# Kernel tuning notes

Hardware: AMD Instinct MI355X
Metric: run time of the kernel (lower is better)

Reference implementation:

```python
import jax, jax.numpy as jnp
import numpy as np

HID = 2048
HEADS = 16
HEAD_DIM = HID // HEADS  # 128
MLP_HID = 4 * HID
L_IMG = 2048
L_TXT = 256


def _layernorm(x, eps=1e-6):
    mu = jnp.mean(x, axis=-1, keepdims=True)
    xc = x - mu
    var = jnp.mean(xc * xc, axis=-1, keepdims=True)
    return xc * jax.lax.rsqrt(var + eps)


def _rmsnorm(x, scale, eps=1e-6):
    xf = x.astype(jnp.float32)
    rrms = jax.lax.rsqrt(jnp.mean(xf * xf, axis=-1, keepdims=True) + eps)
    return (xf * rrms).astype(x.dtype) * scale


def _apply_rope(x, pe):
    # x: [B,H,L,D], pe: [1,1,L,D/2,2,2]
    B, H, L, D = x.shape
    xf = x.astype(jnp.float32).reshape(B, H, L, D // 2, 1, 2)
    out = pe[..., 0] * xf[..., 0] + pe[..., 1] * xf[..., 1]  # [B,H,L,D/2,2]
    return out.reshape(B, H, L, D).astype(x.dtype)


def _attention(q, k, v, pe):
    q = _apply_rope(q, pe)
    k = _apply_rope(k, pe)
    scale = 1.0 / jnp.sqrt(jnp.float32(q.shape[-1])).astype(q.dtype)
    logits = jnp.einsum('bhqd,bhkd->bhqk', q, k) * scale
    probs = jax.nn.softmax(logits, axis=-1)
    out = jnp.einsum('bhqk,bhkd->bhqd', probs, v)
    B, H, L, D = out.shape
    return out.transpose(0, 2, 1, 3).reshape(B, L, H * D)


def _modulation(vec, w, b):
    out = jnp.dot(jax.nn.silu(vec), w) + b  # [B, 6*dim]
    return jnp.split(out[:, None, :], 6, axis=-1)


def _qkv_heads(x, w, b):
    B, L, _ = x.shape
    qkv = (jnp.dot(x, w) + b).reshape(B, L, 3, HEADS, HEAD_DIM)
    qkv = qkv.transpose(2, 0, 3, 1, 4)  # [3,B,H,L,D]
    return qkv[0], qkv[1], qkv[2]


def _mlp(x, w1, b1, w2, b2):
    return jnp.dot(jax.nn.gelu(jnp.dot(x, w1) + b1, approximate=True), w2) + b2


def setup_inputs() -> dict:
    key = jax.random.key(0)
    ks = iter(jax.random.split(key, 32))
    s = 0.02
    d = {
        'img': jax.random.normal(next(ks), (1, L_IMG, HID), jnp.float32),
        'txt': jax.random.normal(next(ks), (1, L_TXT, HID), jnp.float32),
        'vec': jax.random.normal(next(ks), (1, HID), jnp.float32),
        'pe': jax.random.normal(next(ks), (1, 1, L_TXT + L_IMG, HEAD_DIM // 2, 2, 2), jnp.float32),
    }
    for p in ('img', 'txt'):
        d[p + '_mod_w'] = jax.random.normal(next(ks), (HID, 6 * HID), jnp.float32) * s
        d[p + '_mod_b'] = jnp.zeros((6 * HID,), jnp.float32)
        d[p + '_qkv_w'] = jax.random.normal(next(ks), (HID, 3 * HID), jnp.float32) * s
        d[p + '_qkv_b'] = jnp.zeros((3 * HID,), jnp.float32)
        d[p + '_q_scale'] = jnp.ones((HEAD_DIM,), jnp.float32)
        d[p + '_k_scale'] = jnp.ones((HEAD_DIM,), jnp.float32)
        d[p + '_proj_w'] = jax.random.normal(next(ks), (HID, HID), jnp.float32) * s
        d[p + '_proj_b'] = jnp.zeros((HID,), jnp.float32)
        d[p + '_mlp_w1'] = jax.random.normal(next(ks), (HID, MLP_HID), jnp.float32) * s
        d[p + '_mlp_b1'] = jnp.zeros((MLP_HID,), jnp.float32)
        d[p + '_mlp_w2'] = jax.random.normal(next(ks), (MLP_HID, HID), jnp.float32) * s
        d[p + '_mlp_b2'] = jnp.zeros((HID,), jnp.float32)
    return d


def reference(img, txt, vec, pe,
              img_mod_w, img_mod_b, img_qkv_w, img_qkv_b, img_q_scale, img_k_scale,
              img_proj_w, img_proj_b, img_mlp_w1, img_mlp_b1, img_mlp_w2, img_mlp_b2,
              txt_mod_w, txt_mod_b, txt_qkv_w, txt_qkv_b, txt_q_scale, txt_k_scale,
              txt_proj_w, txt_proj_b, txt_mlp_w1, txt_mlp_b1, txt_mlp_w2, txt_mlp_b2):
    i_sh1, i_sc1, i_g1, i_sh2, i_sc2, i_g2 = _modulation(vec, img_mod_w, img_mod_b)
    t_sh1, t_sc1, t_g1, t_sh2, t_sc2, t_g2 = _modulation(vec, txt_mod_w, txt_mod_b)

    img_modulated = (1 + i_sc1) * _layernorm(img) + i_sh1
    iq, ik, iv = _qkv_heads(img_modulated, img_qkv_w, img_qkv_b)
    iq = _rmsnorm(iq, img_q_scale)
    ik = _rmsnorm(ik, img_k_scale)

    txt_modulated = (1 + t_sc1) * _layernorm(txt) + t_sh1
    tq, tk, tv = _qkv_heads(txt_modulated, txt_qkv_w, txt_qkv_b)
    tq = _rmsnorm(tq, txt_q_scale)
    tk = _rmsnorm(tk, txt_k_scale)

    q = jnp.concatenate((tq, iq), axis=2)
    k = jnp.concatenate((tk, ik), axis=2)
    v = jnp.concatenate((tv, iv), axis=2)
    attn = _attention(q, k, v, pe)  # [B, L_txt+L_img, HID]
    Lt = txt.shape[1]
    txt_attn, img_attn = attn[:, :Lt], attn[:, Lt:]

    img = img + i_g1 * (jnp.dot(img_attn, img_proj_w) + img_proj_b)
    img = img + i_g2 * _mlp((1 + i_sc2) * _layernorm(img) + i_sh2,
                            img_mlp_w1, img_mlp_b1, img_mlp_w2, img_mlp_b2)

    txt = txt + t_g1 * (jnp.dot(txt_attn, txt_proj_w) + txt_proj_b)
    txt = txt + t_g2 * _mlp((1 + t_sc2) * _layernorm(txt) + t_sh2,
                            txt_mlp_w1, txt_mlp_b1, txt_mlp_w2, txt_mlp_b2)
    return img, txt
```

## Files before the change

kernel.cpp:

```cpp
#include <hip/hip_runtime.h>
#include <math.h>

typedef unsigned short u16;
typedef short bf16x8 __attribute__((ext_vector_type(8)));
typedef float f32x4 __attribute__((ext_vector_type(4)));

#define HID 2048
#define NH 16
#define HD 128
#define LI 2048
#define LT 256
#define LA 2304
#define MODW 12288

__device__ __forceinline__ u16 f2bf(float f) {
  unsigned int u = __float_as_uint(f);
  u += 0x7fff + ((u >> 16) & 1);
  return (u16)(u >> 16);
}
__device__ __forceinline__ float bf2f(u16 b) {
  return __uint_as_float(((unsigned int)b) << 16);
}

__device__ __forceinline__ void gload16(const void* g, void* l) {
  __builtin_amdgcn_global_load_lds(
      (const __attribute__((address_space(1))) unsigned int*)g,
      (__attribute__((address_space(3))) unsigned int*)l, 16, 0, 0);
}

__global__ void k_mod_partial(const float* __restrict__ vec,
                              const float* __restrict__ wi,
                              const float* __restrict__ wt,
                              float* __restrict__ part) {
  __shared__ float sv[256];
  int j = blockIdx.x * 256 + threadIdx.x;
  int k0 = blockIdx.y * 256;
  const float* w = blockIdx.z ? wt : wi;
  float v = vec[k0 + threadIdx.x];
  sv[threadIdx.x] = v / (1.f + expf(-v));
  __syncthreads();
  float acc = 0.f;
  for (int kk = 0; kk < 256; ++kk)
    acc += sv[kk] * w[(size_t)(k0 + kk) * MODW + j];
  part[(size_t)(blockIdx.z * 8 + blockIdx.y) * MODW + j] = acc;
}

__global__ void k_mod_reduce(const float* __restrict__ part,
                             const float* __restrict__ bi,
                             const float* __restrict__ bt,
                             float* __restrict__ mod) {
  int i = blockIdx.x * 256 + threadIdx.x;
  int s = i / MODW, j = i % MODW;
  const float* b = s ? bt : bi;
  float v = b[j];
#pragma unroll
  for (int c = 0; c < 8; ++c) v += part[(size_t)(s * 8 + c) * MODW + j];
  mod[i] = v;
}

__global__ void k_ln_mod(const float* __restrict__ xi, const float* __restrict__ xt,
                         const float* __restrict__ shi, const float* __restrict__ sci,
                         const float* __restrict__ sht, const float* __restrict__ sct,
                         u16* __restrict__ out) {
  int r = blockIdx.x;
  bool txs = r < LT;
  const float* xr = txs ? (xt + (size_t)r * HID) : (xi + (size_t)(r - LT) * HID);
  const float* sh = txs ? sht : shi;
  const float* sc = txs ? sct : sci;
  float4 v0 = ((const float4*)xr)[threadIdx.x * 2];
  float4 v1 = ((const float4*)xr)[threadIdx.x * 2 + 1];
  float s1 = v0.x + v0.y + v0.z + v0.w + v1.x + v1.y + v1.z + v1.w;
  float s2 = v0.x * v0.x + v0.y * v0.y + v0.z * v0.z + v0.w * v0.w +
             v1.x * v1.x + v1.y * v1.y + v1.z * v1.z + v1.w * v1.w;
#pragma unroll
  for (int m = 1; m < 64; m <<= 1) { s1 += __shfl_xor(s1, m); s2 += __shfl_xor(s2, m); }
  __shared__ float red[8];
  int wid = threadIdx.x >> 6;
  if ((threadIdx.x & 63) == 0) { red[wid] = s1; red[4 + wid] = s2; }
  __syncthreads();
  float tot  = red[0] + red[1] + red[2] + red[3];
  float tot2 = red[4] + red[5] + red[6] + red[7];
  float mu = tot * (1.f / HID);
  float var = tot2 * (1.f / HID) - mu * mu;
  float rs = rsqrtf(var + 1e-6f);
  int c = threadIdx.x * 8;
  float v[8] = {v0.x, v0.y, v0.z, v0.w, v1.x, v1.y, v1.z, v1.w};
  u16 o[8] __attribute__((aligned(16)));
#pragma unroll
  for (int u = 0; u < 8; ++u)
    o[u] = f2bf((v[u] - mu) * rs * (1.f + sc[c + u]) + sh[c + u]);
  *(uint4*)&out[(size_t)r * HID + c] = *(uint4*)o;
}

__global__ void k_tconv(const float* __restrict__ srcI, const float* __restrict__ srcT,
                        u16* __restrict__ dstI, u16* __restrict__ dstT,
                        int K, int N) {
  __shared__ __align__(16) float t[64][65];
  const float* src = blockIdx.z ? srcT : srcI;
  u16* dst = blockIdx.z ? dstT : dstI;
  int n0 = blockIdx.x * 64, k0 = blockIdx.y * 64;
  int tr = threadIdx.x >> 4;
  int tc = (threadIdx.x & 15) * 4;
#pragma unroll
  for (int i = 0; i < 4; ++i) {
    int r = i * 16 + tr;
    float4 v = *(const float4*)&src[(size_t)(k0 + r) * N + n0 + tc];
    t[r][tc] = v.x; t[r][tc + 1] = v.y; t[r][tc + 2] = v.z; t[r][tc + 3] = v.w;
  }
  __syncthreads();
#pragma unroll
  for (int i = 0; i < 4; ++i) {
    int nr = i * 16 + tr;
    ushort4 o;
    o.x = f2bf(t[tc][nr]); o.y = f2bf(t[tc + 1][nr]);
    o.z = f2bf(t[tc + 2][nr]); o.w = f2bf(t[tc + 3][nr]);
    *(ushort4*)&dst[(size_t)(n0 + nr) * K + k0 + tc] = o;
  }
}

template<int MODE>
__global__ __launch_bounds__(256, 4) void k_gemm(
    const u16* __restrict__ A, int lda,
    const u16* __restrict__ B0, const u16* __restrict__ B1, int ldb,
    void* __restrict__ out0, void* __restrict__ out1, int ldc,
    const float* __restrict__ b0, const float* __restrict__ b1, int K,
    const float* __restrict__ x0, const float* __restrict__ x1,
    const float* __restrict__ g0, const float* __restrict__ g1,
    u16* __restrict__ part) {
  __shared__ __align__(16) u16 lA[128 * 64];
  __shared__ __align__(16) u16 lB[128 * 64];
  int gx = gridDim.x, nwg = gx * gridDim.y;
  int bid = blockIdx.y * gx + blockIdx.x;
  int sw = (bid & 7) * (nwg >> 3) + (bid >> 3);
  int by = sw / gx, bx = sw - by * gx;
  int m0 = by * 128, n0 = bx * 128;
  bool txs = (m0 < LT);
  const u16* Bt = txs ? B1 : B0;
  const float* bias = txs ? b1 : b0;
  int mr = txs ? m0 : m0 - LT;
  int z = blockIdx.z;
  int Kh = K / (int)gridDim.z;
  int tid = threadIdx.x, lane = tid & 63, wid = tid >> 6;
  int wh = wid >> 1, ww = wid & 1;
  f32x4 acc[4][4] = {};
  const char* Ab = (const char*)(A + (size_t)m0 * lda + (size_t)z * Kh);
  const char* Bb = (const char*)(Bt + (size_t)n0 * ldb + (size_t)z * Kh);
  int ko = (lane >> 4) * 8, cl = lane & 15;
  for (int k0 = 0; k0 < Kh; k0 += 64) {
#pragma unroll
    for (int i = 0; i < 4; ++i) {
      int o = (i * 256 + tid) * 16;
      int r = o >> 7, cb = o & 127;
      gload16(Ab + (size_t)r * (lda * 2) + k0 * 2 + cb, (char*)lA + o);
      gload16(Bb + (size_t)r * (ldb * 2) + k0 * 2 + cb, (char*)lB + o);
    }
    __syncthreads();
#pragma unroll
    for (int kk = 0; kk < 64; kk += 32) {
      bf16x8 a[4], b[4];
#pragma unroll
      for (int m = 0; m < 4; ++m)
        a[m] = *(const bf16x8*)&lA[(wh * 64 + m * 16 + cl) * 64 + kk + ko];
#pragma unroll
      for (int n = 0; n < 4; ++n)
        b[n] = *(const bf16x8*)&lB[(ww * 64 + n * 16 + cl) * 64 + kk + ko];
#pragma unroll
      for (int m = 0; m < 4; ++m)
#pragma unroll
        for (int n = 0; n < 4; ++n)
          acc[m][n] = __builtin_amdgcn_mfma_f32_16x16x32_bf16(a[m], b[n], acc[m][n], 0, 0, 0);
    }
    __syncthreads();
  }
  int rg = (lane >> 4) * 4;
#pragma unroll
  for (int m = 0; m < 4; ++m) {
    int r0 = wh * 64 + m * 16 + rg;
#pragma unroll
    for (int n = 0; n < 4; ++n) {
      int gcol = n0 + ww * 64 + n * 16 + cl;
#pragma unroll
      for (int j = 0; j < 4; ++j) {
        float v = acc[m][n][j];
        if (MODE == 3) {
          part[(size_t)z * (LA * (size_t)HID) + (size_t)(m0 + r0 + j) * ldc + gcol] = f2bf(v);
        } else {
          v += bias[gcol];
          size_t orow = (size_t)(mr + r0 + j);
          if (MODE == 0) {
            ((float*)(txs ? out1 : out0))[orow * ldc + gcol] = v;
          } else if (MODE == 4) {
            ((u16*)(txs ? out1 : out0))[orow * ldc + gcol] = f2bf(v);
          } else if (MODE == 1) {
            float z2 = 1.5957691216057308f * (v + 0.044715f * v * v * v);
            ((u16*)(txs ? out1 : out0))[orow * ldc + gcol] =
                f2bf(v / (1.f + __expf(-z2)));
          } else {
            const float* xin = txs ? x1 : x0;
            const float* g = txs ? g1 : g0;
            ((float*)(txs ? out1 : out0))[orow * ldc + gcol] =
                xin[orow * ldc + gcol] + g[gcol] * v;
          }
        }
      }
    }
  }
}

template<int NZ>
__global__ void k_red(const u16* __restrict__ P,
                      const float* __restrict__ bias0, const float* __restrict__ bias1,
                      const float* __restrict__ g0, const float* __restrict__ g1,
                      const float* __restrict__ xi, const float* __restrict__ xt,
                      float* __restrict__ oimg, float* __restrict__ otxt) {
  size_t i = ((size_t)blockIdx.x * 256 + threadIdx.x) * 4;
  const size_t S = (size_t)LA * HID;
  int row = (int)(i >> 11), col = (int)(i & (HID - 1));
  float s0 = 0.f, s1 = 0.f, s2 = 0.f, s3 = 0.f;
#pragma unroll
  for (int z = 0; z < NZ; ++z) {
    ushort4 a = *(const ushort4*)&P[i + (size_t)z * S];
    s0 += bf2f(a.x); s1 += bf2f(a.y); s2 += bf2f(a.z); s3 += bf2f(a.w);
  }
  bool txs = row < LT;
  const float* bias = txs ? bias1 : bias0;
  const float* g = txs ? g1 : g0;
  size_t off = txs ? (size_t)row * HID + col : (size_t)(row - LT) * HID + col;
  const float* xin = (txs ? xt : xi) + off;
  float* out = (txs ? otxt : oimg) + off;
  float4 x = *(const float4*)xin;
  float4 o;
  o.x = x.x + g[col] * (s0 + bias[col]);
  o.y = x.y + g[col + 1] * (s1 + bias[col + 1]);
  o.z = x.z + g[col + 2] * (s2 + bias[col + 2]);
  o.w = x.w + g[col + 3] * (s3 + bias[col + 3]);
  *(float4*)out = o;
}

__global__ void k_qkv_post(const u16* __restrict__ qkv,
                           const float* __restrict__ qsi, const float* __restrict__ ksi,
                           const float* __restrict__ qst, const float* __restrict__ kst,
                           const float* __restrict__ pe,
                           u16* __restrict__ Q, u16* __restrict__ K, u16* __restrict__ V) {
  int h = blockIdx.x, lg = blockIdx.y, lane = threadIdx.x;
  bool txs = lg < LT;
  const float* qs = txs ? qst : qsi;
  const float* ks = txs ? kst : ksi;
  const u16* base = qkv + (size_t)lg * 6144 + h * HD;
  float q0 = bf2f(base[2 * lane]), q1 = bf2f(base[2 * lane + 1]);
  float k0 = bf2f(base[2048 + 2 * lane]), k1 = bf2f(base[2048 + 2 * lane + 1]);
  float v0 = bf2f(base[4096 + 2 * lane]), v1 = bf2f(base[4096 + 2 * lane + 1]);
  float sq = q0 * q0 + q1 * q1, sk = k0 * k0 + k1 * k1;
#pragma unroll
  for (int m = 1; m < 64; m <<= 1) { sq += __shfl_xor(sq, m); sk += __shfl_xor(sk, m); }
  float rq = rsqrtf(sq * (1.f / HD) + 1e-6f), rk = rsqrtf(sk * (1.f / HD) + 1e-6f);
  q0 *= rq * qs[2 * lane]; q1 *= rq * qs[2 * lane + 1];
  k0 *= rk * ks[2 * lane]; k1 *= rk * ks[2 * lane + 1];
  float4 p = *(const float4*)&pe[(size_t)lg * 256 + lane * 4];
  float qa = p.x * q0 + p.y * q1, qb = p.z * q0 + p.w * q1;
  float ka = p.x * k0 + p.y * k1, kb = p.z * k0 + p.w * k1;
  size_t ob = ((size_t)h * LA + lg) * HD + 2 * lane;
  Q[ob] = f2bf(qa); Q[ob + 1] = f2bf(qb);
  K[ob] = f2bf(ka); K[ob + 1] = f2bf(kb);
  V[ob] = f2bf(v0); V[ob + 1] = f2bf(v1);
}

__global__ void k_vtrans(const u16* __restrict__ V, u16* __restrict__ Vt) {
  __shared__ __align__(16) u16 t[64][72];
  int l0 = blockIdx.x * 64, d0 = blockIdx.y * 64, h = blockIdx.z;
  const u16* src = V + (size_t)h * LA * HD;
#pragma unroll
  for (int jj = 0; jj < 2; ++jj) {
    int idx = (jj * 256 + threadIdx.x) * 8;
    int r = idx >> 6, c = idx & 63;
    *(uint4*)&t[r][c] = *(const uint4*)&src[(size_t)(l0 + r) * HD + d0 + c];
  }
  __syncthreads();
  u16* dst = Vt + (size_t)h * HD * LA;
#pragma unroll
  for (int jj = 0; jj < 2; ++jj) {
    int idx = (jj * 256 + threadIdx.x) * 8;
    int r = idx >> 6, c = idx & 63;
    u16 o[8] __attribute__((aligned(16)));
#pragma unroll
    for (int u = 0; u < 8; ++u) o[u] = t[c + u][r];
    *(uint4*)&dst[(size_t)(d0 + r) * LA + l0 + c] = *(uint4*)o;
  }
}

__global__ __launch_bounds__(576) void k_flash(
    const u16* __restrict__ Q, const u16* __restrict__ Kg,
    const u16* __restrict__ Vt, u16* __restrict__ attn) {
  __shared__ __align__(16) u16 Ks[2][64 * 128];
  __shared__ __align__(16) u16 Vs[2][128 * 64];
  __shared__ __align__(16) u16 Ps[9][16 * 64];
  int bid = blockIdx.y * gridDim.x + blockIdx.x;
  int xcd = bid & 7, j0 = bid >> 3;
  int h = xcd * 2 + (j0 >> 4);
  int q0 = (j0 & 15) * 144;
  int tid = threadIdx.x, lane = tid & 63, w = tid >> 6;
  int ko = (lane >> 4) * 8, cl = lane & 15;
  const char* Kb = (const char*)(Kg + (size_t)h * LA * HD);
  const char* Vb = (const char*)(Vt + (size_t)h * HD * LA);
  bf16x8 qf[4];
  {
    const u16* Qr = Q + ((size_t)h * LA + q0 + w * 16 + cl) * HD;
#pragma unroll
    for (int kk = 0; kk < 4; ++kk) qf[kk] = *(const bf16x8*)&Qr[kk * 32 + ko];
  }
  f32x4 oacc[8] = {};
  float mst[4] = {-1e30f, -1e30f, -1e30f, -1e30f};
  float lst[4] = {0.f, 0.f, 0.f, 0.f};

  auto stage = [&](int t0, int buf) {
    if (tid < 512) {
#pragma unroll
      for (int i = 0; i < 2; ++i) {
        int o = (i * 512 + tid) * 16;
        int r = o >> 8, c = o & 255;
        gload16(Kb + (size_t)(t0 + r) * 256 + (c ^ ((r & 7) << 4)),
                (char*)Ks[buf] + o);
        int r2 = o >> 7, c2 = o & 127;
        gload16(Vb + (size_t)r2 * (LA * 2) + (size_t)t0 * 2 + (c2 ^ ((r2 & 7) << 4)),
                (char*)Vs[buf] + o);
      }
    }
  };

  stage(0, 0);
  __syncthreads();
  for (int t = 0; t < LA / 64; ++t) {
    int buf = t & 1;
    if (t < LA / 64 - 1) stage((t + 1) * 64, buf ^ 1);
    f32x4 sacc[4] = {};
    __builtin_amdgcn_s_setprio(1);
#pragma unroll
    for (int kk = 0; kk < 4; ++kk) {
      int cb = (kk * 32 + ko) * 2;
#pragma unroll
      for (int n = 0; n < 4; ++n) {
        int row = n * 16 + cl;
        bf16x8 bk = *(const bf16x8*)&Ks[buf][row * 128 + ((cb ^ ((row & 7) << 4)) >> 1)];
        sacc[n] = __builtin_amdgcn_mfma_f32_16x16x32_bf16(qf[kk], bk, sacc[n], 0, 0, 0);
      }
    }
    __builtin_amdgcn_s_setprio(0);
    const float scale = 0.08838834764831845f;
    float mx[4];
#pragma unroll
    for (int j = 0; j < 4; ++j) {
      float m1 = -1e30f;
#pragma unroll
      for (int n = 0; n < 4; ++n) { sacc[n][j] *= scale; m1 = fmaxf(m1, sacc[n][j]); }
#pragma unroll
      for (int m = 1; m < 16; m <<= 1) m1 = fmaxf(m1, __shfl_xor(m1, m));
      mx[j] = m1;
    }
    float dmax = fmaxf(fmaxf(mx[0] - mst[0], mx[1] - mst[1]),
                       fmaxf(mx[2] - mst[2], mx[3] - mst[3]));
    if (!__all(dmax <= 8.f)) {
#pragma unroll
      for (int j = 0; j < 4; ++j) {
        float mnew = fmaxf(mst[j], mx[j]);
        float alpha = __expf(mst[j] - mnew);
        lst[j] *= alpha; mst[j] = mnew;
#pragma unroll
        for (int nd = 0; nd < 8; ++nd) oacc[nd][j] *= alpha;
      }
    }
    float p[4][4];
#pragma unroll
    for (int j = 0; j < 4; ++j) {
      float s = 0.f;
#pragma unroll
      for (int n = 0; n < 4; ++n) { p[n][j] = __expf(sacc[n][j] - mst[j]); s += p[n][j]; }
#pragma unroll
      for (int m = 1; m < 16; m <<= 1) s += __shfl_xor(s, m);
      lst[j] += s;
    }
#pragma unroll
    for (int j = 0; j < 4; ++j) {
      int pr = (lane >> 4) * 4 + j;
#pragma unroll
      for (int n = 0; n < 4; ++n)
        Ps[w][pr * 64 + ((((n * 16 + cl) * 2) ^ ((pr & 7) << 4)) >> 1)] = f2bf(p[n][j]);
    }
    __builtin_amdgcn_s_setprio(1);
#pragma unroll
    for (int kk = 0; kk < 64; kk += 32) {
      int cb = (kk + ko) * 2;
      bf16x8 ap = *(const bf16x8*)&Ps[w][cl * 64 + ((cb ^ ((cl & 7) << 4)) >> 1)];
#pragma unroll
      for (int nd = 0; nd < 8; ++nd) {
        int vr = nd * 16 + cl;
        bf16x8 bv = *(const bf16x8*)&Vs[buf][vr * 64 + ((cb ^ ((vr & 7) << 4)) >> 1)];
        oacc[nd] = __builtin_amdgcn_mfma_f32_16x16x32_bf16(ap, bv, oacc[nd], 0, 0, 0);
      }
    }
    __builtin_amdgcn_s_setprio(0);
    __syncthreads();
  }
#pragma unroll
  for (int j = 0; j < 4; ++j) {
    int lrow = q0 + w * 16 + (lane >> 4) * 4 + j;
    float inv = 1.f / lst[j];
#pragma unroll
    for (int nd = 0; nd < 8; ++nd)
      attn[(size_t)lrow * HID + h * HD + nd * 16 + cl] = f2bf(oacc[nd][j] * inv);
  }
}

extern "C" void kernel_launch(void* const* d_in, const int* in_sizes, int n_in,
                              void* d_out, int out_size, void* d_ws, size_t ws_size,
                              hipStream_t stream) {
  const float* img = (const float*)d_in[0];
  const float* txt = (const float*)d_in[1];
  const float* vec = (const float*)d_in[2];
  const float* pe  = (const float*)d_in[3];
  const float* imod_w = (const float*)d_in[4];
  const float* imod_b = (const float*)d_in[5];
  const float* iqkv_w = (const float*)d_in[6];
  const float* iqkv_b = (const float*)d_in[7];
  const float* iq_s   = (const float*)d_in[8];
  const float* ik_s   = (const float*)d_in[9];
  const float* iproj_w = (const float*)d_in[10];
  const float* iproj_b = (const float*)d_in[11];
  const float* imlp_w1 = (const float*)d_in[12];
  const float* imlp_b1 = (const float*)d_in[13];
  const float* imlp_w2 = (const float*)d_in[14];
  const float* imlp_b2 = (const float*)d_in[15];
  const float* tmod_w = (const float*)d_in[16];
  const float* tmod_b = (const float*)d_in[17];
  const float* tqkv_w = (const float*)d_in[18];
  const float* tqkv_b = (const float*)d_in[19];
  const float* tq_s   = (const float*)d_in[20];
  const float* tk_s   = (const float*)d_in[21];
  const float* tproj_w = (const float*)d_in[22];
  const float* tproj_b = (const float*)d_in[23];
  const float* tmlp_w1 = (const float*)d_in[24];
  const float* tmlp_b1 = (const float*)d_in[25];
  const float* tmlp_w2 = (const float*)d_in[26];
  const float* tmlp_b2 = (const float*)d_in[27];
  (void)in_sizes; (void)n_in; (void)out_size; (void)ws_size;

  float* oimg = (float*)d_out;
  float* otxt = oimg + (size_t)LI * HID;

  char* p = (char*)d_ws;
  auto alloc = [&](size_t b) { char* r = p; p += (b + 255) & ~(size_t)255; return r; };
  float* part = (float*)alloc((size_t)16 * MODW * 4);
  float* mod  = (float*)alloc((size_t)2 * MODW * 4);
  u16*  xm    = (u16*)alloc((size_t)LA * HID * 2);
  u16*  wt_i  = (u16*)alloc((size_t)8192 * 2048 * 2);
  u16*  wt_t  = (u16*)alloc((size_t)8192 * 2048 * 2);
  u16*  qkvr  = (u16*)alloc((size_t)LA * 6144 * 2);
  u16*  Qb    = (u16*)alloc((size_t)NH * LA * HD * 2);
  u16*  Kb    = (u16*)alloc((size_t)NH * LA * HD * 2);
  u16*  Vb    = (u16*)alloc((size_t)NH * LA * HD * 2);
  u16*  Vtb   = (u16*)alloc((size_t)NH * LA * HD * 2);
  u16*  attn  = (u16*)alloc((size_t)LA * HID * 2);
  u16*  hb    = (u16*)alloc((size_t)LA * 8192 * 2);
  u16*  kpart = (u16*)alloc((size_t)4 * LA * HID * 2);

  const float* MI = mod;
  const float* MT = mod + MODW;

  k_mod_partial<<<dim3(48, 8, 2), 256, 0, stream>>>(vec, imod_w, tmod_w, part);
  k_mod_reduce<<<dim3(96), 256, 0, stream>>>(part, imod_b, tmod_b, mod);

  k_ln_mod<<<dim3(LA), 256, 0, stream>>>(img, txt, MI, MI + 2048, MT, MT + 2048, xm);

  k_tconv<<<dim3(96, 32, 2), 256, 0, stream>>>(iqkv_w, tqkv_w, wt_i, wt_t, 2048, 6144);
  k_gemm<4><<<dim3(48, 18), 256, 0, stream>>>(xm, 2048, wt_i, wt_t, 2048,
      qkvr + (size_t)LT * 6144, qkvr, 6144, iqkv_b, tqkv_b, 2048,
      nullptr, nullptr, nullptr, nullptr, nullptr);

  k_qkv_post<<<dim3(NH, LA), 64, 0, stream>>>(qkvr, iq_s, ik_s, tq_s, tk_s, pe, Qb, Kb, Vb);
  k_vtrans<<<dim3(36, 2, NH), 256, 0, stream>>>(Vb, Vtb);

  k_flash<<<dim3(16, NH), 576, 0, stream>>>(Qb, Kb, Vtb, attn);

  k_tconv<<<dim3(32, 32, 2), 256, 0, stream>>>(iproj_w, tproj_w, wt_i, wt_t, 2048, 2048);
  k_gemm<2><<<dim3(16, 18), 256, 0, stream>>>(attn, 2048, wt_i, wt_t, 2048,
      oimg, otxt, 2048, iproj_b, tproj_b, 2048,
      img, txt, MI + 4096, MT + 4096, nullptr);

  k_ln_mod<<<dim3(LA), 256, 0, stream>>>(oimg, otxt, MI + 6144, MI + 8192,
                                         MT + 6144, MT + 8192, xm);

  k_tconv<<<dim3(128, 32, 2), 256, 0, stream>>>(imlp_w1, tmlp_w1, wt_i, wt_t, 2048, 8192);
  k_gemm<1><<<dim3(64, 18), 256, 0, stream>>>(xm, 2048, wt_i, wt_t, 2048,
      hb + (size_t)LT * 8192, hb, 8192, imlp_b1, tmlp_b1, 2048,
      nullptr, nullptr, nullptr, nullptr, nullptr);

  k_tconv<<<dim3(32, 128, 2), 256, 0, stream>>>(imlp_w2, tmlp_w2, wt_i, wt_t, 8192, 2048);
  k_gemm<3><<<dim3(16, 18, 4), 256, 0, stream>>>(hb, 8192, wt_i, wt_t, 8192,
      nullptr, nullptr, 2048, nullptr, nullptr, 8192,
      nullptr, nullptr, nullptr, nullptr, kpart);
  k_red<4><<<dim3(4608), 256, 0, stream>>>(kpart, imlp_b2, tmlp_b2,
      MI + 10240, MT + 10240, oimg, otxt, oimg, otxt);
}
```

Baseline: 656.1 us.

## Use 256x256-tile double-buffered GEMM kernel for QKV projection

Adds a new GEMM kernel with 256x256 output tiles, 512 threads, double-buffered LDS, and global loads for the next K-tile interleaved between MFMA groups. It replaces the 128-tile GEMM for the QKV projection only. Larger tiles raise arithmetic intensity and cut redundant global loads, and the staging overlaps memory with compute. The cost is a grid of only 216 workgroups at one block per CU, which leaves the 256-CU device underfilled and lowers occupancy.

```diff
diff --git a/kernel.cpp b/kernel.cpp
--- a/kernel.cpp
+++ b/kernel.cpp
@@ -115,6 +115,107 @@
     o.x = f2bf(t[tc][nr]); o.y = f2bf(t[tc + 1][nr]);
     o.z = f2bf(t[tc + 2][nr]); o.w = f2bf(t[tc + 3][nr]);
     *(ushort4*)&dst[(size_t)(n0 + nr) * K + k0 + tc] = o;
+  }
+}
+
+__global__ __launch_bounds__(512, 1) void k_gemm256q(
+    const u16* __restrict__ A, int lda,
+    const u16* __restrict__ B0, const u16* __restrict__ B1, int ldb,
+    u16* __restrict__ out0, u16* __restrict__ out1, int ldc,
+    const float* __restrict__ b0, const float* __restrict__ b1, int K) {
+  __shared__ __align__(16) u16 lA[2][256 * 64];
+  __shared__ __align__(16) u16 lB[2][256 * 64];
+  int gx = gridDim.x, nwg = gx * gridDim.y;
+  int bid = blockIdx.y * gx + blockIdx.x;
+  int sw = (bid & 7) * (nwg >> 3) + (bid >> 3);
+  int by = sw / gx, bx = sw - by * gx;
+  int m0 = by * 256, n0 = bx * 256;
+  bool txs = (m0 == 0);
+  const u16* Bt = txs ? B1 : B0;
+  const float* bias = txs ? b1 : b0;
+  int mr = txs ? 0 : m0 - LT;
+  int tid = threadIdx.x, lane = tid & 63, w = tid >> 6;
+  int wm = w >> 2, wn = w & 3;
+  int cl = lane & 15, ko2 = (lane >> 4) * 16;
+  f32x4 acc[8][4] = {};
+  const char* Ab = (const char*)A + (size_t)m0 * lda * 2;
+  const char* Bb = (const char*)Bt + (size_t)n0 * ldb * 2;
+  int NT = K >> 6;
+
+  auto stageHalf = [&](int g, int q, int which) {
+    const char* base = (which < 2) ? Ab : Bb;
+    int ld2 = ((which < 2) ? lda : ldb) * 2;
+    int rbase = (which & 1) * 128;
+    char* dst = ((which < 2) ? (char*)lA[q] : (char*)lB[q]) + rbase * 128;
+#pragma unroll
+    for (int i = 0; i < 2; ++i) {
+      int o = (i * 512 + tid) * 16;
+      int r = o >> 7, c = o & 127;
+      gload16(base + (size_t)(rbase + r) * ld2 + g * 128 + (c ^ ((r & 7) << 4)),
+              dst + o);
+    }
+  };
+  bf16x8 a[4], b[4];
+  auto ldA4 = [&](int q, int mh, int kk) {
+    int cb = kk * 64 + ko2;
+#pragma unroll
+    for (int i = 0; i < 4; ++i) {
+      int row = wm * 128 + mh * 64 + i * 16 + cl;
+      a[i] = *(const bf16x8*)((const char*)lA[q] + row * 128 + (cb ^ ((row & 7) << 4)));
+    }
+  };
+  auto ldB4 = [&](int q, int kk) {
+    int cb = kk * 64 + ko2;
+#pragma unroll
+    for (int nf = 0; nf < 4; ++nf) {
+      int row = wn * 64 + nf * 16 + cl;
+      b[nf] = *(const bf16x8*)((const char*)lB[q] + row * 128 + (cb ^ ((row & 7) << 4)));
+    }
+  };
+  auto mf16 = [&](int mh) {
+    asm volatile("s_waitcnt lgkmcnt(0)" ::: "memory");
+    __builtin_amdgcn_sched_barrier(0);
+    __builtin_amdgcn_s_setprio(1);
+#pragma unroll
+    for (int i = 0; i < 4; ++i)
+#pragma unroll
+      for (int nf = 0; nf < 4; ++nf)
+        acc[mh * 4 + i][nf] = __builtin_amdgcn_mfma_f32_16x16x32_bf16(
+            a[i], b[nf], acc[mh * 4 + i][nf], 0, 0, 0);
+    __builtin_amdgcn_s_setprio(0);
+    __builtin_amdgcn_sched_barrier(0);
+  };
+
+  stageHalf(0, 0, 0); stageHalf(0, 0, 1); stageHalf(0, 0, 2); stageHalf(0, 0, 3);
+  for (int g = 0; g < NT; ++g) {
+    int q = g & 1;
+    bool pre = (g + 1 < NT);
+    asm volatile("s_waitcnt vmcnt(0)" ::: "memory");
+    __builtin_amdgcn_s_barrier();
+    if (pre) stageHalf(g + 1, q ^ 1, 0);
+    ldA4(q, 0, 0); ldB4(q, 0); mf16(0);
+    if (pre) stageHalf(g + 1, q ^ 1, 1);
+    ldA4(q, 1, 0); mf16(1);
+    if (pre) stageHalf(g + 1, q ^ 1, 2);
+    ldA4(q, 0, 1); ldB4(q, 1); mf16(0);
+    if (pre) stageHalf(g + 1, q ^ 1, 3);
+    ldA4(q, 1, 1); mf16(1);
+  }
+
+  int rg = (lane >> 4) * 4;
+#pragma unroll
+  for (int mf = 0; mf < 8; ++mf) {
+    int r0 = wm * 128 + mf * 16 + rg;
+#pragma unroll
+    for (int nf = 0; nf < 4; ++nf) {
+      int gcol = n0 + wn * 64 + nf * 16 + cl;
+      float bv = bias[gcol];
+#pragma unroll
+      for (int j = 0; j < 4; ++j) {
+        size_t orow = (size_t)(mr + r0 + j);
+        (txs ? out1 : out0)[orow * ldc + gcol] = f2bf(acc[mf][nf][j] + bv);
+      }
+    }
   }
 }
 
@@ -471,9 +572,8 @@
   k_ln_mod<<<dim3(LA), 256, 0, stream>>>(img, txt, MI, MI + 2048, MT, MT + 2048, xm);
 
   k_tconv<<<dim3(96, 32, 2), 256, 0, stream>>>(iqkv_w, tqkv_w, wt_i, wt_t, 2048, 6144);
-  k_gemm<4><<<dim3(48, 18), 256, 0, stream>>>(xm, 2048, wt_i, wt_t, 2048,
-      qkvr + (size_t)LT * 6144, qkvr, 6144, iqkv_b, tqkv_b, 2048,
-      nullptr, nullptr, nullptr, nullptr, nullptr);
+  k_gemm256q<<<dim3(24, 9), 512, 0, stream>>>(xm, 2048, wt_i, wt_t, 2048,
+      qkvr + (size_t)LT * 6144, qkvr, 6144, iqkv_b, tqkv_b, 2048);
 
   k_qkv_post<<<dim3(NH, LA), 64, 0, stream>>>(qkvr, iq_s, ik_s, tq_s, tk_s, pe, Qb, Kb, Vb);
   k_vtrans<<<dim3(36, 2, NH), 256, 0, stream>>>(Vb, Vtb);
```

After: 660.0 us. About the same (+0.6%).
